# Optimization experiments

Measured on AMD Instinct MI355X. Metric: run time of the kernel, lower is better.

The kernel has to match this reference:

```python
import jax, jax.numpy as jnp
import numpy as np

REG_MAX = 16
BOX_W = 7.5
OBJ_W = 1.0
TOPK = 10
EPS = 1e-7


def dfl_decode(x, reg_max):
    # x: [B, 4*reg_max, N] -> expected value of per-side distribution -> [B, N, 4] (xyxy)
    B, C, N = x.shape
    x = x.reshape(B, 4, reg_max, N)
    p = jax.nn.softmax(x, axis=2)
    proj = jnp.arange(reg_max, dtype=x.dtype)
    return jnp.einsum('bkrn,r->bnk', p, proj)


def bbox_ciou(b1, b2):
    # b1: [B,N,1,4], b2: [B,1,M,4], xyxy -> [B,N,M]
    x11, y11, x12, y12 = b1[..., 0], b1[..., 1], b1[..., 2], b1[..., 3]
    x21, y21, x22, y22 = b2[..., 0], b2[..., 1], b2[..., 2], b2[..., 3]
    w1, h1 = x12 - x11, y12 - y11
    w2, h2 = x22 - x21, y22 - y21
    iw = jnp.clip(jnp.minimum(x12, x22) - jnp.maximum(x11, x21), 0.0)
    ih = jnp.clip(jnp.minimum(y12, y22) - jnp.maximum(y11, y21), 0.0)
    inter = iw * ih
    union = w1 * h1 + w2 * h2 - inter + EPS
    iou = inter / union
    cw = jnp.maximum(x12, x22) - jnp.minimum(x11, x21)
    ch = jnp.maximum(y12, y22) - jnp.minimum(y11, y21)
    c2 = cw * cw + ch * ch + EPS
    rho2 = ((x21 + x22 - x11 - x12) ** 2 + (y21 + y22 - y11 - y12) ** 2) * 0.25
    v = (4.0 / (np.pi ** 2)) * (jnp.arctan(w2 / (h2 + EPS)) - jnp.arctan(w1 / (h1 + EPS))) ** 2
    alpha = jax.lax.stop_gradient(v / (v - iou + 1.0 + EPS))
    return iou - rho2 / c2 - alpha * v


def setup_inputs() -> dict:
    key = jax.random.key(0)
    k1, k2, k3, k4 = jax.random.split(key, 4)
    B, N, M = 8, 34000, 64
    boxes = jax.random.normal(k1, (B, 4 * REG_MAX, N), dtype=jnp.float32)
    scores = jax.random.normal(k2, (B, N), dtype=jnp.float32)
    # GT boxes: valid xyxy in roughly the same [0, reg_max) range as decoded preds
    xy = jax.random.uniform(k3, (B, M, 2), dtype=jnp.float32) * 11.0
    wh = jax.random.uniform(k4, (B, M, 2), dtype=jnp.float32) * 4.0 + 0.5
    targets = jnp.concatenate([xy, xy + wh], axis=-1)
    return {'boxes': boxes, 'scores': scores, 'targets': targets}


def reference(boxes, scores, targets):
    B, N = scores.shape
    M = targets.shape[1]
    pb = dfl_decode(boxes, REG_MAX)                     # [B,N,4]
    ciou = bbox_ciou(pb[:, :, None, :], targets[:, None, :, :])  # [B,N,M]
    k = min(TOPK, N)
    topv, topi = jax.lax.top_k(jnp.swapaxes(ciou, 1, 2), k)      # [B,M,k] over anchors
    valid = topv > 0.0
    vals = jnp.where(valid, topv, 0.0)

    def per_batch(idx, val, vld):
        flat_i = idx.reshape(-1)
        iou_t = jnp.zeros((N,), val.dtype).at[flat_i].max(val.reshape(-1))
        pos = jnp.zeros((N,), bool).at[flat_i].max(vld.reshape(-1))
        return iou_t, pos

    iou_target, pos = jax.vmap(per_batch)(topi, vals, valid)     # [B,N]
    posf = pos.astype(iou_target.dtype)
    npos = posf.sum(axis=1)
    box_per = jnp.where(npos > 0,
                        ((1.0 - iou_target) * posf).sum(axis=1) / jnp.maximum(npos, 1.0),
                        0.0)
    box_loss = box_per.sum()
    # BCEWithLogits (mean over anchors), summed over batch
    bce = jnp.maximum(scores, 0.0) - scores * iou_target + jnp.log1p(jnp.exp(-jnp.abs(scores)))
    obj_loss = bce.mean(axis=1).sum()
    total = (BOX_W * box_loss + OBJ_W * obj_loss) / B
    return total, box_loss, obj_loss
```

## Files before the change

kernel.cpp:

```cpp
#include <hip/hip_runtime.h>
#include <math.h>

#define BQ 8
#define MQ 64
#define KTOP 10
#define EPSQ 1e-7f
#define APBA 256
#define CHUNK 512
#define MBUF 1344

__device__ __forceinline__ float frcp(float x) { return __builtin_amdgcn_rcpf(x); }

__device__ __forceinline__ float dfl_side(const float* __restrict__ p, size_t Ns) {
  float x0 = p[0];
  float x1 = p[Ns];
  float x2 = p[2 * Ns];
  float x3 = p[3 * Ns];
  float x4 = p[4 * Ns];
  float x5 = p[5 * Ns];
  float x6 = p[6 * Ns];
  float x7 = p[7 * Ns];
  float x8 = p[8 * Ns];
  float x9 = p[9 * Ns];
  float x10 = p[10 * Ns];
  float x11 = p[11 * Ns];
  float x12 = p[12 * Ns];
  float x13 = p[13 * Ns];
  float x14 = p[14 * Ns];
  float x15 = p[15 * Ns];
  float mx = fmaxf(fmaxf(fmaxf(fmaxf(x0, x1), fmaxf(x2, x3)),
                         fmaxf(fmaxf(x4, x5), fmaxf(x6, x7))),
                   fmaxf(fmaxf(fmaxf(x8, x9), fmaxf(x10, x11)),
                         fmaxf(fmaxf(x12, x13), fmaxf(x14, x15))));
  float s = 0.f, ws = 0.f, e;
  e = __expf(x0 - mx); s += e;
  e = __expf(x1 - mx); s += e; ws += 1.f * e;
  e = __expf(x2 - mx); s += e; ws += 2.f * e;
  e = __expf(x3 - mx); s += e; ws += 3.f * e;
  e = __expf(x4 - mx); s += e; ws += 4.f * e;
  e = __expf(x5 - mx); s += e; ws += 5.f * e;
  e = __expf(x6 - mx); s += e; ws += 6.f * e;
  e = __expf(x7 - mx); s += e; ws += 7.f * e;
  e = __expf(x8 - mx); s += e; ws += 8.f * e;
  e = __expf(x9 - mx); s += e; ws += 9.f * e;
  e = __expf(x10 - mx); s += e; ws += 10.f * e;
  e = __expf(x11 - mx); s += e; ws += 11.f * e;
  e = __expf(x12 - mx); s += e; ws += 12.f * e;
  e = __expf(x13 - mx); s += e; ws += 13.f * e;
  e = __expf(x14 - mx); s += e; ws += 14.f * e;
  e = __expf(x15 - mx); s += e; ws += 15.f * e;
  return ws * frcp(s);
}

__global__ __launch_bounds__(256) void decode_kernel(
    const float* __restrict__ boxes, const float* __restrict__ scores,
    float4* __restrict__ ev4, unsigned int* __restrict__ iou_bits,
    float* __restrict__ bcePartial, unsigned int* __restrict__ ctr,
    int N, int bpbA) {
  const int tid = threadIdx.x;
  const int b = blockIdx.x / bpbA;
  const int blk = blockIdx.x - b * bpbA;
  const int n = blk * APBA + tid;
  const int w = tid >> 6;
  const int l = tid & 63;
  if (blockIdx.x == 0 && tid == 0) *ctr = 0u;

  float bce0 = 0.f;
  if (n < N) {
    const size_t i = (size_t)b * N + n;
    iou_bits[i] = 0u;
    float sc = scores[i];
    bce0 = fmaxf(sc, 0.f) + log1pf(__expf(-fabsf(sc)));
    const size_t Ns = (size_t)N;
    const float* base = boxes + (size_t)(b * 64) * Ns + n;
    float e0 = dfl_side(base, Ns);
    float e1 = dfl_side(base + 16 * Ns, Ns);
    float e2 = dfl_side(base + 32 * Ns, Ns);
    float e3 = dfl_side(base + 48 * Ns, Ns);
    ev4[i] = make_float4(e0, e1, e2, e3);
  }
#pragma unroll
  for (int d = 1; d < 64; d <<= 1) bce0 += __shfl_xor(bce0, d, 64);
  if (l == 0) bcePartial[blockIdx.x * 4 + w] = bce0;
}

__global__ __launch_bounds__(256) void topk_kernel(
    const float4* __restrict__ ev4, const float* __restrict__ targets,
    uint2* __restrict__ cand, int N, int bpbB) {
  const int tid = threadIdx.x;
  const int b = blockIdx.x / bpbB;
  const int blk = blockIdx.x - b * bpbB;
  const int c0 = blk * CHUNK;
  const int w = tid >> 6;
  const int l = tid & 63;

  __shared__ float4 s_sv[CHUNK];
  __shared__ float s_at[CHUNK];
  __shared__ int s_ix[CHUNK];
  __shared__ float s_hv[4 * MQ * KTOP];
  __shared__ int s_hi[4 * MQ * KTOP];
  __shared__ uint2 s_mg[MQ * KTOP];
  __shared__ int s_cnt;
  if (tid == 0) s_cnt = 0;
  __syncthreads();

#pragma unroll
  for (int p = 0; p < CHUNK / 256; ++p) {
    const int n = c0 + p * 256 + tid;
    bool pred = false;
    float4 ev = make_float4(0.f, 0.f, 0.f, 0.f);
    float at = 0.f;
    if (n < N) {
      ev = ev4[(size_t)b * N + n];
      float w1 = ev.z - ev.x, h1 = ev.w - ev.y;
      if (w1 > 0.f && h1 > 0.f) {
        pred = true;
        at = atanf(w1 * frcp(h1 + EPSQ));
      }
    }
    unsigned long long mask = __ballot(pred);
    int cnt = __popcll(mask);
    int bslot = 0;
    if (l == 0 && cnt) bslot = atomicAdd(&s_cnt, cnt);
    bslot = __shfl(bslot, 0, 64);
    if (pred) {
      int pos = bslot + __popcll(mask & ((1ull << l) - 1ull));
      s_sv[pos] = ev;
      s_at[pos] = at;
      s_ix[pos] = n;
    }
  }
  __syncthreads();
  const int nsurv = s_cnt;

  const float4 t = ((const float4*)targets)[b * MQ + l];
  const float x21 = t.x, y21 = t.y, x22 = t.z, y22 = t.w;
  const float w2 = x22 - x21, h2 = y22 - y21;
  const float atan_t = atanf(w2 * frcp(h2 + EPSQ));
  const float area2 = w2 * h2, sumx2 = x21 + x22, sumy2 = y21 + y22;
  const float CPI = 4.0f / (float)(M_PI * M_PI);

  float hv0 = 0.f, hv1 = 0.f, hv2 = 0.f, hv3 = 0.f, hv4 = 0.f;
  float hv5 = 0.f, hv6 = 0.f, hv7 = 0.f, hv8 = 0.f, hv9 = 0.f;
  int hi0 = 0, hi1 = 0, hi2 = 0, hi3 = 0, hi4 = 0;
  int hi5 = 0, hi6 = 0, hi7 = 0, hi8 = 0, hi9 = 0;

  const int qlen = (nsurv + 3) >> 2;
  const int j0 = w * qlen;
  const int j1 = min(nsurv, j0 + qlen);
  for (int j = j0; j < j1; ++j) {
    float4 p = s_sv[j];
    float pa = s_at[j];
    int ixj = s_ix[j];
    float x11 = p.x, y11 = p.y, x12 = p.z, y12 = p.w;
    float w1 = x12 - x11, h1 = y12 - y11;
    float iw = fmaxf(fminf(x12, x22) - fmaxf(x11, x21), 0.f);
    float ih = fmaxf(fminf(y12, y22) - fmaxf(y11, y21), 0.f);
    float inter = iw * ih;
    float uni = w1 * h1 + area2 - inter + EPSQ;
    float iou = inter * frcp(uni);
    float cw = fmaxf(x12, x22) - fminf(x11, x21);
    float ch = fmaxf(y12, y22) - fminf(y11, y21);
    float c2 = cw * cw + ch * ch + EPSQ;
    float dx = sumx2 - x11 - x12;
    float dy = sumy2 - y11 - y12;
    float rho2 = (dx * dx + dy * dy) * 0.25f;
    float da = atan_t - pa;
    float v = CPI * da * da;
    float alpha = v * frcp(v - iou + 1.f + EPSQ);
    float ciou = iou - rho2 * frcp(c2) - alpha * v;
    if (ciou > hv9) {
      float cv = ciou;
      int ci = ixj;
#define INS(vk, ik)                         \
  {                                         \
    bool gt = cv > vk;                      \
    float tv_ = vk; int ti_ = ik;           \
    vk = gt ? cv : vk; ik = gt ? ci : ik;   \
    cv = gt ? tv_ : cv; ci = gt ? ti_ : ci; \
  }
      INS(hv0, hi0) INS(hv1, hi1) INS(hv2, hi2) INS(hv3, hi3) INS(hv4, hi4)
      INS(hv5, hi5) INS(hv6, hi6) INS(hv7, hi7) INS(hv8, hi8) INS(hv9, hi9)
#undef INS
    }
  }
  const int hb = (w * MQ + l) * KTOP;
  s_hv[hb + 0] = hv0; s_hi[hb + 0] = hi0;
  s_hv[hb + 1] = hv1; s_hi[hb + 1] = hi1;
  s_hv[hb + 2] = hv2; s_hi[hb + 2] = hi2;
  s_hv[hb + 3] = hv3; s_hi[hb + 3] = hi3;
  s_hv[hb + 4] = hv4; s_hi[hb + 4] = hi4;
  s_hv[hb + 5] = hv5; s_hi[hb + 5] = hi5;
  s_hv[hb + 6] = hv6; s_hi[hb + 6] = hi6;
  s_hv[hb + 7] = hv7; s_hi[hb + 7] = hi7;
  s_hv[hb + 8] = hv8; s_hi[hb + 8] = hi8;
  s_hv[hb + 9] = hv9; s_hi[hb + 9] = hi9;
  __syncthreads();

  if (w == 0) {
    const int m = l;
    int p0 = 0, p1 = 0, p2 = 0, p3 = 0;
    for (int r = 0; r < KTOP; ++r) {
      float c0v = s_hv[(0 * MQ + m) * KTOP + p0];
      float c1 = s_hv[(1 * MQ + m) * KTOP + p1];
      float c2m = s_hv[(2 * MQ + m) * KTOP + p2];
      float c3 = s_hv[(3 * MQ + m) * KTOP + p3];
      float best = c0v; int bw = 0;
      if (c1 > best) { best = c1; bw = 1; }
      if (c2m > best) { best = c2m; bw = 2; }
      if (c3 > best) { best = c3; bw = 3; }
      int psel = (bw == 0) ? p0 : (bw == 1) ? p1 : (bw == 2) ? p2 : p3;
      int bidx = s_hi[(bw * MQ + m) * KTOP + psel];
      s_mg[m * KTOP + r] = make_uint2(__float_as_uint(best), (unsigned)bidx);
      if (bw == 0) p0 = min(p0 + 1, KTOP - 1);
      else if (bw == 1) p1 = min(p1 + 1, KTOP - 1);
      else if (bw == 2) p2 = min(p2 + 1, KTOP - 1);
      else p3 = min(p3 + 1, KTOP - 1);
    }
  }
  __syncthreads();
  uint2* obase = cand + (size_t)(b * bpbB + blk) * (MQ * KTOP);
  for (int sl = tid; sl < MQ * KTOP; sl += 256) obase[sl] = s_mg[sl];
}

__device__ __forceinline__ void select_top10(
    float* s_bv, int* s_bi, float* s_winv, int* s_wini,
    int* s_cnt, int c, int tid) {
  if (tid < 64) {
    for (int r = 0; r < KTOP; ++r) {
      float bv = 0.f;
      int bs = 0xffff;
      for (int sl = tid; sl < c; sl += 64) {
        float v = s_bv[sl];
        if (v > bv) { bv = v; bs = sl; }
      }
      unsigned long long key =
          ((unsigned long long)__float_as_uint(bv) << 32) | (unsigned int)bs;
#pragma unroll
      for (int d = 1; d < 64; d <<= 1) {
        unsigned long long o = __shfl_xor(key, d, 64);
        if (o > key) key = o;
      }
      if (tid == 0) {
        float wv = __uint_as_float((unsigned int)(key >> 32));
        int ws = (int)(key & 0xffffu);
        s_winv[r] = wv;
        if (wv > 0.f && ws != 0xffff) {
          s_wini[r] = s_bi[ws];
          s_bv[ws] = 0.f;
        } else {
          s_wini[r] = 0;
        }
      }
    }
    if (tid < KTOP) { s_bv[tid] = s_winv[tid]; s_bi[tid] = s_wini[tid]; }
    if (tid == 0) *s_cnt = KTOP;
  }
}

__global__ __launch_bounds__(256) void merge_kernel(
    const uint2* __restrict__ cand, const float* __restrict__ scores,
    unsigned int* __restrict__ iou_bits, const float* __restrict__ bcePartial,
    float* __restrict__ mergePartial, unsigned int* __restrict__ ctr,
    float* __restrict__ out, int N, int bpbB, int bpbA) {
  const int bm = blockIdx.x;
  const int b = bm >> 6;
  const int m = bm & 63;
  const int tid = threadIdx.x;
  const int l = tid & 63;
  const int NC = bpbB * KTOP;

  __shared__ float s_bv[MBUF];
  __shared__ int s_bi[MBUF];
  __shared__ float s_winv[KTOP];
  __shared__ int s_wini[KTOP];
  __shared__ int s_cnt;
  __shared__ float s_d[3];
  __shared__ int s_last;
  __shared__ float s_acc[BQ * 3];
  if (tid == 0) s_cnt = 0;
  if (tid < 3) s_d[tid] = 0.f;
  if (tid < BQ * 3) s_acc[tid] = 0.f;
  __syncthreads();

  for (int k2 = tid; k2 < NC; k2 += 256) {
    int blkk = k2 / KTOP;
    int r = k2 - blkk * KTOP;
    uint2 e = cand[((size_t)(b * bpbB + blkk) * MQ + m) * KTOP + r];
    float v = __uint_as_float(e.x);
    bool p = v > 0.f;
    unsigned long long mask = __ballot(p);
    int cnt = __popcll(mask);
    int bslot = 0;
    if (l == 0 && cnt) bslot = atomicAdd(&s_cnt, cnt);
    bslot = __shfl(bslot, 0, 64);
    if (p) {
      int pos = bslot + __popcll(mask & ((1ull << l) - 1ull));
      s_bv[pos] = v;
      s_bi[pos] = (int)e.y;
    }
  }
  __syncthreads();
  int c = s_cnt;
  __syncthreads();
  if (c > KTOP) {
    select_top10(s_bv, s_bi, s_winv, s_wini, &s_cnt, c, tid);
    __syncthreads();
    c = KTOP;
  }
  if (tid < KTOP && tid < c) {
    float v = s_bv[tid];
    if (v > 0.f) {
      int ix = s_bi[tid];
      unsigned int vb = __float_as_uint(v);
      unsigned int old = atomicMax(&iou_bits[(size_t)b * N + ix], vb);
      if (old < vb) {
        float vold = __uint_as_float(old);
        bool was = (old != 0u);
        atomicAdd(&s_d[0], was ? (vold - v) : (1.f - v));
        if (!was) atomicAdd(&s_d[1], 1.f);
        atomicAdd(&s_d[2], -scores[(size_t)b * N + ix] * (v - vold));
      }
    }
  }
  __syncthreads();
  if (tid == 0) {
    float4* mp = (float4*)(mergePartial + (size_t)bm * 4);
    *mp = make_float4(s_d[0], s_d[1], s_d[2], 0.f);
    __threadfence();
    unsigned int done = atomicAdd(ctr, 1u);
    s_last = (done == (unsigned)(gridDim.x - 1)) ? 1 : 0;
  }
  __syncthreads();
  if (s_last) {
    __threadfence();
    volatile const float* mp = mergePartial;
    for (int i = tid; i < BQ * MQ; i += 256) {
      int bb = i >> 6;
      float a0 = mp[i * 4 + 0];
      float a1 = mp[i * 4 + 1];
      float a2 = mp[i * 4 + 2];
      atomicAdd(&s_acc[bb * 3 + 0], a0);
      atomicAdd(&s_acc[bb * 3 + 1], a1);
      atomicAdd(&s_acc[bb * 3 + 2], a2);
    }
    volatile const float* bp = bcePartial;
    const int per_b = bpbA * 4;
    for (int i = tid; i < BQ * per_b; i += 256) {
      int bb = i / per_b;
      atomicAdd(&s_acc[bb * 3 + 2], bp[i]);
    }
    __syncthreads();
    if (tid == 0) {
      float box = 0.f, obj = 0.f;
      for (int bb = 0; bb < BQ; ++bb) {
        float np = s_acc[bb * 3 + 1];
        box += (np > 0.f) ? s_acc[bb * 3 + 0] / fmaxf(np, 1.f) : 0.f;
        obj += s_acc[bb * 3 + 2] / (float)N;
      }
      out[0] = (7.5f * box + obj) / (float)BQ;
      out[1] = box;
      out[2] = obj;
    }
  }
}

extern "C" void kernel_launch(void* const* d_in, const int* in_sizes, int n_in,
                              void* d_out, int out_size, void* d_ws, size_t ws_size,
                              hipStream_t stream) {
  const float* boxes = (const float*)d_in[0];
  const float* scores = (const float*)d_in[1];
  const float* targets = (const float*)d_in[2];
  float* out = (float*)d_out;
  const int N = in_sizes[1] / BQ;

  const int bpbA = (N + APBA - 1) / APBA;
  const int nblkA = BQ * bpbA;
  const int bpbB = (N + CHUNK - 1) / CHUNK;
  const int nblkB = BQ * bpbB;

  char* ws = (char*)d_ws;
  size_t ev_bytes = (size_t)BQ * N * sizeof(float4);
  size_t cand_bytes = (size_t)BQ * bpbB * MQ * KTOP * sizeof(uint2);
  size_t iou_bytes = (size_t)BQ * N * sizeof(unsigned int);
  size_t bce_bytes = (((size_t)nblkA * 4 * sizeof(float)) + 255) & ~(size_t)255;
  size_t mp_bytes = (size_t)BQ * MQ * 4 * sizeof(float);

  float4* ev4 = (float4*)ws;                   ws += ev_bytes;
  uint2* cand = (uint2*)ws;                    ws += cand_bytes;
  unsigned int* iou_bits = (unsigned int*)ws;  ws += iou_bytes;
  float* bcePartial = (float*)ws;              ws += bce_bytes;
  float* mergePartial = (float*)ws;            ws += mp_bytes;
  unsigned int* ctr = (unsigned int*)ws;

  decode_kernel<<<nblkA, 256, 0, stream>>>(boxes, scores, ev4, iou_bits,
                                           bcePartial, ctr, N, bpbA);
  topk_kernel<<<nblkB, 256, 0, stream>>>(ev4, targets, cand, N, bpbB);
  merge_kernel<<<BQ * MQ, 256, 0, stream>>>(cand, scores, iou_bits, bcePartial,
                                            mergePartial, ctr, out, N, bpbB, bpbA);
}
```

Measured before the change: 147.9 us.

## Split DFL decode per side with async global-to-LDS tile loads and SoA output

The decode kernel now gives each block one box side over a 1024-anchor chunk. Its 16 distribution rows are staged into a 64KB shared-memory tile with `global_load_lds` direct loads, so the scores/BCE work can overlap the copy. The decoded values are written as four separate planes (structure-of-arrays) instead of float4, and the top-k kernel reads four scalars per anchor. This aims to improve load concurrency and parallelism in the decode stage. The large LDS tile limits blocks per CU, and the SoA layout adds three extra load streams in top-k.

```diff
diff --git a/kernel.cpp b/kernel.cpp
--- a/kernel.cpp
+++ b/kernel.cpp
@@ -5,98 +5,116 @@
 #define MQ 64
 #define KTOP 10
 #define EPSQ 1e-7f
-#define APBA 256
-#define CHUNK 512
+#define CHUNKA 1024
+#define CHUNKB 512
 #define MBUF 1344
 
 __device__ __forceinline__ float frcp(float x) { return __builtin_amdgcn_rcpf(x); }
-
-__device__ __forceinline__ float dfl_side(const float* __restrict__ p, size_t Ns) {
-  float x0 = p[0];
-  float x1 = p[Ns];
-  float x2 = p[2 * Ns];
-  float x3 = p[3 * Ns];
-  float x4 = p[4 * Ns];
-  float x5 = p[5 * Ns];
-  float x6 = p[6 * Ns];
-  float x7 = p[7 * Ns];
-  float x8 = p[8 * Ns];
-  float x9 = p[9 * Ns];
-  float x10 = p[10 * Ns];
-  float x11 = p[11 * Ns];
-  float x12 = p[12 * Ns];
-  float x13 = p[13 * Ns];
-  float x14 = p[14 * Ns];
-  float x15 = p[15 * Ns];
-  float mx = fmaxf(fmaxf(fmaxf(fmaxf(x0, x1), fmaxf(x2, x3)),
-                         fmaxf(fmaxf(x4, x5), fmaxf(x6, x7))),
-                   fmaxf(fmaxf(fmaxf(x8, x9), fmaxf(x10, x11)),
-                         fmaxf(fmaxf(x12, x13), fmaxf(x14, x15))));
-  float s = 0.f, ws = 0.f, e;
-  e = __expf(x0 - mx); s += e;
-  e = __expf(x1 - mx); s += e; ws += 1.f * e;
-  e = __expf(x2 - mx); s += e; ws += 2.f * e;
-  e = __expf(x3 - mx); s += e; ws += 3.f * e;
-  e = __expf(x4 - mx); s += e; ws += 4.f * e;
-  e = __expf(x5 - mx); s += e; ws += 5.f * e;
-  e = __expf(x6 - mx); s += e; ws += 6.f * e;
-  e = __expf(x7 - mx); s += e; ws += 7.f * e;
-  e = __expf(x8 - mx); s += e; ws += 8.f * e;
-  e = __expf(x9 - mx); s += e; ws += 9.f * e;
-  e = __expf(x10 - mx); s += e; ws += 10.f * e;
-  e = __expf(x11 - mx); s += e; ws += 11.f * e;
-  e = __expf(x12 - mx); s += e; ws += 12.f * e;
-  e = __expf(x13 - mx); s += e; ws += 13.f * e;
-  e = __expf(x14 - mx); s += e; ws += 14.f * e;
-  e = __expf(x15 - mx); s += e; ws += 15.f * e;
-  return ws * frcp(s);
-}
 
 __global__ __launch_bounds__(256) void decode_kernel(
     const float* __restrict__ boxes, const float* __restrict__ scores,
-    float4* __restrict__ ev4, unsigned int* __restrict__ iou_bits,
-    float* __restrict__ bcePartial, unsigned int* __restrict__ ctr,
-    int N, int bpbA) {
+    float* __restrict__ evs,
+    unsigned int* __restrict__ iou_bits, float* __restrict__ bcePartial,
+    unsigned int* __restrict__ ctr, int N, int nchunk) {
   const int tid = threadIdx.x;
-  const int b = blockIdx.x / bpbA;
-  const int blk = blockIdx.x - b * bpbA;
-  const int n = blk * APBA + tid;
   const int w = tid >> 6;
   const int l = tid & 63;
+  int t = blockIdx.x;
+  const int c = t % nchunk;
+  t /= nchunk;
+  const int s = t & 3;
+  const int b = t >> 2;
+  const int c0 = c * CHUNKA;
+
+  __shared__ __align__(16) float tile[16][CHUNKA];
+
   if (blockIdx.x == 0 && tid == 0) *ctr = 0u;
 
+  const size_t Ns = (size_t)N;
+  const size_t BN = (size_t)BQ * N;
+
+#pragma unroll
+  for (int rr = 0; rr < 4; ++rr) {
+    const int r = 4 * w + rr;
+    const float* rowg = boxes + (size_t)(b * 64 + s * 16 + r) * Ns;
+#pragma unroll
+    for (int k = 0; k < 4; ++k) {
+      int fi = c0 + k * 256 + l * 4;
+      if (fi > N - 4) fi = N - 4;
+      __builtin_amdgcn_global_load_lds(
+          (const __attribute__((address_space(1))) void*)(rowg + fi),
+          (__attribute__((address_space(3))) void*)&tile[r][k * 256],
+          16, 0, 0);
+    }
+  }
   float bce0 = 0.f;
-  if (n < N) {
-    const size_t i = (size_t)b * N + n;
-    iou_bits[i] = 0u;
-    float sc = scores[i];
-    bce0 = fmaxf(sc, 0.f) + log1pf(__expf(-fabsf(sc)));
-    const size_t Ns = (size_t)N;
-    const float* base = boxes + (size_t)(b * 64) * Ns + n;
-    float e0 = dfl_side(base, Ns);
-    float e1 = dfl_side(base + 16 * Ns, Ns);
-    float e2 = dfl_side(base + 32 * Ns, Ns);
-    float e3 = dfl_side(base + 48 * Ns, Ns);
-    ev4[i] = make_float4(e0, e1, e2, e3);
-  }
-#pragma unroll
-  for (int d = 1; d < 64; d <<= 1) bce0 += __shfl_xor(bce0, d, 64);
-  if (l == 0) bcePartial[blockIdx.x * 4 + w] = bce0;
+  if (s == 0) {
+#pragma unroll
+    for (int p = 0; p < 4; ++p) {
+      const int n = c0 + p * 256 + tid;
+      if (n < N) {
+        const size_t i = (size_t)b * N + n;
+        iou_bits[i] = 0u;
+        float sc = scores[i];
+        bce0 += fmaxf(sc, 0.f) + log1pf(__expf(-fabsf(sc)));
+      }
+    }
+#pragma unroll
+    for (int d = 1; d < 64; d <<= 1) bce0 += __shfl_xor(bce0, d, 64);
+    if (l == 0) bcePartial[(size_t)(b * nchunk + c) * 4 + w] = bce0;
+  }
+  asm volatile("s_waitcnt vmcnt(0)" ::: "memory");
+  __syncthreads();
+
+#pragma unroll
+  for (int p = 0; p < 4; ++p) {
+    const int col = p * 256 + tid;
+    const int n = c0 + col;
+    float x0 = tile[0][col], x1 = tile[1][col], x2 = tile[2][col],
+          x3 = tile[3][col], x4 = tile[4][col], x5 = tile[5][col],
+          x6 = tile[6][col], x7 = tile[7][col], x8 = tile[8][col],
+          x9 = tile[9][col], x10 = tile[10][col], x11 = tile[11][col],
+          x12 = tile[12][col], x13 = tile[13][col], x14 = tile[14][col],
+          x15 = tile[15][col];
+    float mx = fmaxf(fmaxf(fmaxf(fmaxf(x0, x1), fmaxf(x2, x3)),
+                           fmaxf(fmaxf(x4, x5), fmaxf(x6, x7))),
+                     fmaxf(fmaxf(fmaxf(x8, x9), fmaxf(x10, x11)),
+                           fmaxf(fmaxf(x12, x13), fmaxf(x14, x15))));
+    float sm = 0.f, ws = 0.f, e;
+    e = __expf(x0 - mx); sm += e;
+    e = __expf(x1 - mx); sm += e; ws += 1.f * e;
+    e = __expf(x2 - mx); sm += e; ws += 2.f * e;
+    e = __expf(x3 - mx); sm += e; ws += 3.f * e;
+    e = __expf(x4 - mx); sm += e; ws += 4.f * e;
+    e = __expf(x5 - mx); sm += e; ws += 5.f * e;
+    e = __expf(x6 - mx); sm += e; ws += 6.f * e;
+    e = __expf(x7 - mx); sm += e; ws += 7.f * e;
+    e = __expf(x8 - mx); sm += e; ws += 8.f * e;
+    e = __expf(x9 - mx); sm += e; ws += 9.f * e;
+    e = __expf(x10 - mx); sm += e; ws += 10.f * e;
+    e = __expf(x11 - mx); sm += e; ws += 11.f * e;
+    e = __expf(x12 - mx); sm += e; ws += 12.f * e;
+    e = __expf(x13 - mx); sm += e; ws += 13.f * e;
+    e = __expf(x14 - mx); sm += e; ws += 14.f * e;
+    e = __expf(x15 - mx); sm += e; ws += 15.f * e;
+    if (n < N) evs[(size_t)s * BN + (size_t)b * N + n] = ws * frcp(sm);
+  }
 }
 
 __global__ __launch_bounds__(256) void topk_kernel(
-    const float4* __restrict__ ev4, const float* __restrict__ targets,
+    const float* __restrict__ evs, const float* __restrict__ targets,
     uint2* __restrict__ cand, int N, int bpbB) {
   const int tid = threadIdx.x;
   const int b = blockIdx.x / bpbB;
   const int blk = blockIdx.x - b * bpbB;
-  const int c0 = blk * CHUNK;
+  const int c0 = blk * CHUNKB;
   const int w = tid >> 6;
   const int l = tid & 63;
-
-  __shared__ float4 s_sv[CHUNK];
-  __shared__ float s_at[CHUNK];
-  __shared__ int s_ix[CHUNK];
+  const size_t BN = (size_t)BQ * N;
+
+  __shared__ float4 s_sv[CHUNKB];
+  __shared__ float s_at[CHUNKB];
+  __shared__ int s_ix[CHUNKB];
   __shared__ float s_hv[4 * MQ * KTOP];
   __shared__ int s_hi[4 * MQ * KTOP];
   __shared__ uint2 s_mg[MQ * KTOP];
@@ -105,13 +123,17 @@
   __syncthreads();
 
 #pragma unroll
-  for (int p = 0; p < CHUNK / 256; ++p) {
+  for (int p = 0; p < CHUNKB / 256; ++p) {
     const int n = c0 + p * 256 + tid;
     bool pred = false;
     float4 ev = make_float4(0.f, 0.f, 0.f, 0.f);
     float at = 0.f;
     if (n < N) {
-      ev = ev4[(size_t)b * N + n];
+      const size_t i = (size_t)b * N + n;
+      ev.x = evs[0 * BN + i];
+      ev.y = evs[1 * BN + i];
+      ev.z = evs[2 * BN + i];
+      ev.w = evs[3 * BN + i];
       float w1 = ev.z - ev.x, h1 = ev.w - ev.y;
       if (w1 > 0.f && h1 > 0.f) {
         pred = true;
@@ -262,7 +284,7 @@
     const uint2* __restrict__ cand, const float* __restrict__ scores,
     unsigned int* __restrict__ iou_bits, const float* __restrict__ bcePartial,
     float* __restrict__ mergePartial, unsigned int* __restrict__ ctr,
-    float* __restrict__ out, int N, int bpbB, int bpbA) {
+    float* __restrict__ out, int N, int bpbB, int nchunk) {
   const int bm = blockIdx.x;
   const int b = bm >> 6;
   const int m = bm & 63;
@@ -345,7 +367,7 @@
       atomicAdd(&s_acc[bb * 3 + 2], a2);
     }
     volatile const float* bp = bcePartial;
-    const int per_b = bpbA * 4;
+    const int per_b = nchunk * 4;
     for (int i = tid; i < BQ * per_b; i += 256) {
       int bb = i / per_b;
       atomicAdd(&s_acc[bb * 3 + 2], bp[i]);
@@ -374,28 +396,28 @@
   float* out = (float*)d_out;
   const int N = in_sizes[1] / BQ;
 
-  const int bpbA = (N + APBA - 1) / APBA;
-  const int nblkA = BQ * bpbA;
-  const int bpbB = (N + CHUNK - 1) / CHUNK;
+  const int nchunk = (N + CHUNKA - 1) / CHUNKA;
+  const int nblkA = BQ * 4 * nchunk;
+  const int bpbB = (N + CHUNKB - 1) / CHUNKB;
   const int nblkB = BQ * bpbB;
 
   char* ws = (char*)d_ws;
-  size_t ev_bytes = (size_t)BQ * N * sizeof(float4);
+  size_t evs_bytes = (size_t)4 * BQ * N * sizeof(float);
   size_t cand_bytes = (size_t)BQ * bpbB * MQ * KTOP * sizeof(uint2);
   size_t iou_bytes = (size_t)BQ * N * sizeof(unsigned int);
-  size_t bce_bytes = (((size_t)nblkA * 4 * sizeof(float)) + 255) & ~(size_t)255;
+  size_t bce_bytes = (((size_t)BQ * nchunk * 4 * sizeof(float)) + 255) & ~(size_t)255;
   size_t mp_bytes = (size_t)BQ * MQ * 4 * sizeof(float);
 
-  float4* ev4 = (float4*)ws;                   ws += ev_bytes;
+  float* evs = (float*)ws;                     ws += evs_bytes;
   uint2* cand = (uint2*)ws;                    ws += cand_bytes;
   unsigned int* iou_bits = (unsigned int*)ws;  ws += iou_bytes;
   float* bcePartial = (float*)ws;              ws += bce_bytes;
   float* mergePartial = (float*)ws;            ws += mp_bytes;
   unsigned int* ctr = (unsigned int*)ws;
 
-  decode_kernel<<<nblkA, 256, 0, stream>>>(boxes, scores, ev4, iou_bits,
-                                           bcePartial, ctr, N, bpbA);
-  topk_kernel<<<nblkB, 256, 0, stream>>>(ev4, targets, cand, N, bpbB);
+  decode_kernel<<<nblkA, 256, 0, stream>>>(boxes, scores, evs, iou_bits,
+                                           bcePartial, ctr, N, nchunk);
+  topk_kernel<<<nblkB, 256, 0, stream>>>(evs, targets, cand, N, bpbB);
   merge_kernel<<<BQ * MQ, 256, 0, stream>>>(cand, scores, iou_bits, bcePartial,
-                                            mergePartial, ctr, out, N, bpbB, bpbA);
+                                            mergePartial, ctr, out, N, bpbB, nchunk);
 }
```

After: 143.9 us. -2.7%, faster.
